# Kernel optimization log

Measured on AMD Instinct MI355X. Metric: run time of the kernel, lower is better.

Reference implementation:

```python
import jax, jax.numpy as jnp
import numpy as np

N = 50000        # num nodes
E = 800000       # num edges (before self loops)
IN = 256         # in_channels
H = 4            # heads
C = 32           # out_channels per head
NEG_SLOPE = 0.2


def _glorot(key, shape):
    fan = shape[-2] * (shape[-1] if len(shape) > 2 else 1) + shape[-1]
    # PyG glorot: uniform(-s, s) with s = sqrt(6 / (fan_in + fan_out))
    s = float(np.sqrt(6.0 / (shape[-2] + shape[-1])))
    return jax.random.uniform(key, shape, jnp.float32, -s, s)


def setup_inputs() -> dict:
    key = jax.random.key(0)
    k1, k2, k3, k4, k5 = jax.random.split(key, 5)
    x = jax.random.normal(k1, (N, IN), jnp.float32)
    src = jax.random.randint(k2, (E,), 0, N)
    dst = jax.random.randint(k3, (E,), 0, N)
    # guarantee no self loops (module removes them then re-adds exactly N loops)
    dst = jnp.where(dst == src, (dst + 1) % N, dst)
    edge_index = jnp.stack([src, dst]).astype(jnp.int32)
    weight = _glorot(k4, (IN, H * C))
    att = _glorot(k5, (1, H, 2 * C))
    bias = jnp.zeros((H * C,), jnp.float32)
    return {"x": x, "weight": weight, "att": att, "bias": bias,
            "edge_index": edge_index}


def reference(x, weight, att, bias, edge_index):
    n = x.shape[0]
    # linear projection -> [N, H, C]
    h = (x @ weight).reshape(n, H, C)
    # add self loops (input edge_index has none)
    loops = jnp.arange(n, dtype=edge_index.dtype)
    ei = jnp.concatenate([edge_index, jnp.stack([loops, loops])], axis=1)
    src, dst = ei[0], ei[1]          # flow source_to_target: j=src(row 0), i=dst(row 1)
    x_j = h[src]                     # [E', H, C] source features
    x_i = h[dst]                     # [E', H, C] target features
    wl = att[:, :, :C]               # applied to x_i (first half of concat)
    wr = att[:, :, C:]               # applied to x_j
    alpha = (x_i * wl).sum(-1) + (x_j * wr).sum(-1)   # [E', H]
    alpha = jax.nn.leaky_relu(alpha, NEG_SLOPE)
    # NOTE: module normalizes softmax over edge_index[0] (src) segments
    seg = src
    amax = jax.ops.segment_max(alpha, seg, num_segments=n)
    alpha = jnp.exp(alpha - amax[seg])
    denom = jax.ops.segment_sum(alpha, seg, num_segments=n)
    alpha = alpha / (denom[seg] + 1e-16)
    # weighted messages, aggregated at edge_index[i] = edge_index[1] (dst)
    msg = x_j * alpha[:, :, None]                     # [E', H, C]
    out = jax.ops.segment_sum(msg, dst, num_segments=n)  # [N, H, C]
    return out.reshape(n, H * C) + bias
```

## Files before the change

### kernel.cpp

```cpp
#include <hip/hip_runtime.h>
#include <hip/hip_fp16.h>
#include <math.h>


#define NH 4
#define CH 32
#define HC 128
#define IND 256
#define NEG_SLOPE 0.2f
#define CSH 8
#define NCB_MAX 256
#define CHUNK 4096

typedef __attribute__((ext_vector_type(8))) short bf16x8;
typedef __attribute__((ext_vector_type(16))) float f32x16;

__device__ __forceinline__ unsigned short f2bf(float f) {
    unsigned int u = __float_as_uint(f);
    unsigned int r = (u + 0x7FFFu + ((u >> 16) & 1u)) >> 16;
    return (unsigned short)r;
}
__device__ __forceinline__ float bf2f(unsigned short s) {
    return __uint_as_float(((unsigned int)s) << 16);
}

__global__ __launch_bounds__(256) void k_init0(int* __restrict__ histS,
                                               int* __restrict__ histD, int ncb) {
    int t = threadIdx.x;
    if (t < ncb) { histS[t] = 0; histD[t] = 0; }
}

__global__ __launch_bounds__(256) void k_wprep(const float* __restrict__ W,
                                               unsigned short* __restrict__ WT_bf) {
    int t = blockIdx.x * 256 + threadIdx.x;
    if (t >= IND * HC) return;
    int c = t >> 8;
    int k = t & 255;
    WT_bf[t] = f2bf(W[k * HC + c]);
}

__global__ __launch_bounds__(256) void k_gemm_mfma(const float* __restrict__ x,
                                                   const unsigned short* __restrict__ WT_bf,
                                                   const float* __restrict__ att,
                                                   unsigned short* __restrict__ h_bf,
                                                   float* __restrict__ al,
                                                   float* __restrict__ ar, int N) {
    __shared__ float cs[128 * 129];
    unsigned short* wsT = (unsigned short*)cs;

    const int tid  = threadIdx.x;
    const int row0 = blockIdx.x * 128;
    const int wave = tid >> 6;
    const int lane = tid & 63;
    const int n32  = lane & 31;
    const int half = lane >> 5;

    {
        int c  = tid >> 1;
        int kh = (tid & 1) * 128;
        const unsigned short* src = WT_bf + c * IND + kh;
        unsigned short* dst = wsT + c * 258 + kh;
#pragma unroll
        for (int j = 0; j < 128; j += 8)
            *(int4*)(dst + j) = *(const int4*)(src + j);
    }
    __syncthreads();

    const int row   = row0 + wave * 32 + n32;
    const bool valid = row < N;
    const float* xrow = x + (size_t)row * IND + half * 8;

    f32x16 acc[4];
#pragma unroll
    for (int t = 0; t < 4; t++)
#pragma unroll
        for (int r = 0; r < 16; r++) acc[t][r] = 0.0f;

#pragma unroll 4
    for (int s = 0; s < 16; s++) {
        float4 v0 = make_float4(0.f, 0.f, 0.f, 0.f);
        float4 v1 = v0;
        if (valid) {
            v0 = *(const float4*)(xrow + s * 16);
            v1 = *(const float4*)(xrow + s * 16 + 4);
        }
        bf16x8 a;
        a[0] = (short)f2bf(v0.x); a[1] = (short)f2bf(v0.y);
        a[2] = (short)f2bf(v0.z); a[3] = (short)f2bf(v0.w);
        a[4] = (short)f2bf(v1.x); a[5] = (short)f2bf(v1.y);
        a[6] = (short)f2bf(v1.z); a[7] = (short)f2bf(v1.w);
#pragma unroll
        for (int t = 0; t < 4; t++) {
            bf16x8 b = *(const bf16x8*)(wsT + (t * 32 + n32) * 258 + s * 16 + half * 8);
            acc[t] = __builtin_amdgcn_mfma_f32_32x32x16_bf16(a, b, acc[t], 0, 0, 0);
        }
    }
    __syncthreads();

#pragma unroll
    for (int t = 0; t < 4; t++)
#pragma unroll
        for (int r = 0; r < 16; r++) {
            int rl = wave * 32 + (r & 3) + 8 * (r >> 2) + 4 * half;
            cs[rl * 129 + t * 32 + n32] = acc[t][r];
        }
    __syncthreads();

    const int rl   = tid >> 1;
    const int chf  = tid & 1;
    const int orow = row0 + rl;
    if (orow < N) {
        const float* cr = cs + rl * 129 + chf * 64;
        unsigned short* hp = h_bf + (size_t)orow * HC + chf * 64;
#pragma unroll
        for (int c = 0; c < 64; c += 8) {
            ushort4 o0, o1;
            o0.x = f2bf(cr[c]);     o0.y = f2bf(cr[c + 1]);
            o0.z = f2bf(cr[c + 2]); o0.w = f2bf(cr[c + 3]);
            o1.x = f2bf(cr[c + 4]); o1.y = f2bf(cr[c + 5]);
            o1.z = f2bf(cr[c + 6]); o1.w = f2bf(cr[c + 7]);
            *(ushort4*)(hp + c) = o0;
            *(ushort4*)(hp + c + 4) = o1;
        }
        const int h0 = 2 * chf, h1 = 2 * chf + 1;
        const float* w0 = att + h0 * (2 * CH);
        const float* w1 = att + h1 * (2 * CH);
        float sl0 = 0.f, sr0 = 0.f, sl1 = 0.f, sr1 = 0.f;
#pragma unroll
        for (int c = 0; c < CH; c++) {
            float v0 = cr[c];
            float v1 = cr[CH + c];
            sl0 += v0 * w0[c];  sr0 += v0 * w0[CH + c];
            sl1 += v1 * w1[c];  sr1 += v1 * w1[CH + c];
        }
        al[orow * NH + h0] = sl0;  al[orow * NH + h1] = sl1;
        ar[orow * NH + h0] = sr0;  ar[orow * NH + h1] = sr1;
    }
}

__global__ __launch_bounds__(256) void k_hist(const int* __restrict__ ei,
                                              int* __restrict__ histS,
                                              int* __restrict__ histD,
                                              int E, int NE, int ncb) {
    __shared__ int hs[NCB_MAX], hd[NCB_MAX];
    hs[threadIdx.x] = 0; hd[threadIdx.x] = 0;
    __syncthreads();
    for (int t = blockIdx.x * 256 + threadIdx.x; t < NE; t += gridDim.x * 256) {
        int src, dst;
        if (t < E) { src = ei[t]; dst = ei[E + t]; }
        else       { src = dst = t - E; }
        atomicAdd(&hs[src >> CSH], 1);
        atomicAdd(&hd[dst >> CSH], 1);
    }
    __syncthreads();
    int i = threadIdx.x;
    if (i < ncb) {
        if (hs[i]) atomicAdd(&histS[i], hs[i]);
        if (hd[i]) atomicAdd(&histD[i], hd[i]);
    }
}

__global__ __launch_bounds__(256) void k_scanC(const int* __restrict__ histS,
                                               const int* __restrict__ histD,
                                               int* __restrict__ baseS,
                                               int* __restrict__ baseD,
                                               int* __restrict__ curS,
                                               int* __restrict__ curD,
                                               int* __restrict__ rowptrS,
                                               int* __restrict__ rowptrD,
                                               int ncb, int NE, int N) {
    __shared__ int sc[256];
    int tid = threadIdx.x;
    int v = (tid < ncb) ? histS[tid] : 0;
    sc[tid] = v;
    __syncthreads();
    for (int o = 1; o < 256; o <<= 1) {
        int t = (tid >= o) ? sc[tid - o] : 0;
        __syncthreads();
        sc[tid] += t;
        __syncthreads();
    }
    if (tid < ncb) { baseS[tid] = sc[tid] - v; curS[tid] = sc[tid] - v; }
    if (tid == 0) { baseS[ncb] = sc[255]; rowptrS[N] = NE; }
    __syncthreads();
    v = (tid < ncb) ? histD[tid] : 0;
    sc[tid] = v;
    __syncthreads();
    for (int o = 1; o < 256; o <<= 1) {
        int t = (tid >= o) ? sc[tid - o] : 0;
        __syncthreads();
        sc[tid] += t;
        __syncthreads();
    }
    if (tid < ncb) { baseD[tid] = sc[tid] - v; curD[tid] = sc[tid] - v; }
    if (tid == 0) { baseD[ncb] = sc[255]; rowptrD[N] = NE; }
}

__global__ __launch_bounds__(256) void k_scatterC(const int* __restrict__ ei,
                                                  int* __restrict__ gcurS,
                                                  int* __restrict__ gcurD,
                                                  unsigned int* __restrict__ recS,
                                                  unsigned int* __restrict__ recD,
                                                  int E, int NE, int ncb) {
    __shared__ unsigned int srt[CHUNK];
    __shared__ int cnt[NCB_MAX], off[NCB_MAX], cur[NCB_MAX], gpos[NCB_MAX], sc[256];
    const int tid = threadIdx.x;
    const int t0  = blockIdx.x * CHUNK;
    const int m   = min(CHUNK, NE - t0);

    unsigned int myrec[CHUNK / 256];
    int nmy = 0;
    for (int i = tid; i < m; i += 256) {
        int t = t0 + i;
        int src, dst;
        if (t < E) { src = ei[t]; dst = ei[E + t]; }
        else       { src = dst = t - E; }
        myrec[nmy++] = (unsigned int)src | ((unsigned int)dst << 16);
    }

    for (int side = 0; side < 2; side++) {
        cnt[tid] = 0;
        __syncthreads();
        int mybkt[CHUNK / 256];
        for (int k = 0; k < nmy; k++) {
            unsigned int r = myrec[k];
            int node = side ? (int)(r >> 16) : (int)(r & 0xFFFFu);
            mybkt[k] = node >> CSH;
            atomicAdd(&cnt[mybkt[k]], 1);
        }
        __syncthreads();
        int v = cnt[tid];
        sc[tid] = v;
        __syncthreads();
        for (int o = 1; o < 256; o <<= 1) {
            int t = (tid >= o) ? sc[tid - o] : 0;
            __syncthreads();
            sc[tid] += t;
            __syncthreads();
        }
        off[tid] = sc[tid] - v;
        cur[tid] = sc[tid] - v;
        __syncthreads();
        for (int k = 0; k < nmy; k++) {
            int p = atomicAdd(&cur[mybkt[k]], 1);
            srt[p] = myrec[k];
        }
        __syncthreads();
        int* gcur = side ? gcurD : gcurS;
        if (tid < ncb) {
            int c = cnt[tid];
            gpos[tid] = c ? atomicAdd(&gcur[tid], c) : 0;
        }
        __syncthreads();
        unsigned int* recX = side ? recD : recS;
        for (int i = tid; i < m; i += 256) {
            unsigned int r = srt[i];
            int node = side ? (int)(r >> 16) : (int)(r & 0xFFFFu);
            int cb = node >> CSH;
            recX[gpos[cb] + (i - off[cb])] = r;
        }
        __syncthreads();
    }
}

__global__ __launch_bounds__(256) void k_rebin(const unsigned int* __restrict__ recS,
                                               const unsigned int* __restrict__ recD,
                                               const int* __restrict__ baseS,
                                               const int* __restrict__ baseD,
                                               unsigned short* __restrict__ adjS,
                                               unsigned short* __restrict__ adjD,
                                               int* __restrict__ rowptrS,
                                               int* __restrict__ rowptrD,
                                               int ncb, int N) {
    __shared__ int cnt[256], cur[256], sc[256];
    const int tid  = threadIdx.x;
    const int side = (blockIdx.x >= ncb) ? 1 : 0;
    const int cb   = side ? blockIdx.x - ncb : blockIdx.x;
    const unsigned int* rec = side ? recD : recS;
    const int* base = side ? baseD : baseS;
    const int b0 = base[cb], b1 = base[cb + 1];
    const int tot_rec = b1 - b0;

    cnt[tid] = 0;
    __syncthreads();
    for (int i = tid; i < tot_rec; i += 256) {
        unsigned int r = rec[b0 + i];
        int node = side ? (int)(r >> 16) : (int)(r & 0xFFFFu);
        atomicAdd(&cnt[node & 255], 1);
    }
    __syncthreads();
    int v = cnt[tid];
    sc[tid] = v;
    __syncthreads();
    for (int o = 1; o < 256; o <<= 1) {
        int t = (tid >= o) ? sc[tid - o] : 0;
        __syncthreads();
        sc[tid] += t;
        __syncthreads();
    }
    int ex = sc[tid] - v;
    int node_g = (cb << CSH) + tid;
    int* rowptr = side ? rowptrD : rowptrS;
    if (node_g < N) rowptr[node_g] = b0 + ex;
    cur[tid] = ex;
    __syncthreads();
    unsigned short* adj = side ? adjD : adjS;
    for (int i = tid; i < tot_rec; i += 256) {
        unsigned int r = rec[b0 + i];
        int node = side ? (int)(r >> 16) : (int)(r & 0xFFFFu);
        unsigned short other = side ? (unsigned short)(r & 0xFFFFu)
                                    : (unsigned short)(r >> 16);
        int p = atomicAdd(&cur[node & 255], 1);
        adj[b0 + p] = other;
    }
}

__global__ __launch_bounds__(256) void k_denom(const int* __restrict__ rowptrS,
                                               const unsigned short* __restrict__ adjS,
                                               const float* __restrict__ al,
                                               const float* __restrict__ ar,
                                               float* __restrict__ rdenom, int N) {
    int n = blockIdx.x * 256 + threadIdx.x;
    if (n >= N) return;
    int beg = rowptrS[n], end = rowptrS[n + 1];
    float4 arv = *(const float4*)(ar + n * NH);
    float s0 = 0.f, s1 = 0.f, s2 = 0.f, s3 = 0.f;
    int i = beg;
    for (; i + 2 <= end; i += 2) {
        int d0 = adjS[i], d1 = adjS[i + 1];
        float4 av0 = *(const float4*)(al + d0 * NH);
        float4 av1 = *(const float4*)(al + d1 * NH);
        float a0 = av0.x + arv.x, a1 = av0.y + arv.y;
        float a2 = av0.z + arv.z, a3 = av0.w + arv.w;
        float c0 = av1.x + arv.x, c1 = av1.y + arv.y;
        float c2 = av1.z + arv.z, c3 = av1.w + arv.w;
        a0 = (a0 > 0.f) ? a0 : NEG_SLOPE * a0;
        a1 = (a1 > 0.f) ? a1 : NEG_SLOPE * a1;
        a2 = (a2 > 0.f) ? a2 : NEG_SLOPE * a2;
        a3 = (a3 > 0.f) ? a3 : NEG_SLOPE * a3;
        c0 = (c0 > 0.f) ? c0 : NEG_SLOPE * c0;
        c1 = (c1 > 0.f) ? c1 : NEG_SLOPE * c1;
        c2 = (c2 > 0.f) ? c2 : NEG_SLOPE * c2;
        c3 = (c3 > 0.f) ? c3 : NEG_SLOPE * c3;
        s0 += __expf(a0) + __expf(c0);
        s1 += __expf(a1) + __expf(c1);
        s2 += __expf(a2) + __expf(c2);
        s3 += __expf(a3) + __expf(c3);
    }
    if (i < end) {
        int d0 = adjS[i];
        float4 av = *(const float4*)(al + d0 * NH);
        float a0 = av.x + arv.x, a1 = av.y + arv.y;
        float a2 = av.z + arv.z, a3 = av.w + arv.w;
        a0 = (a0 > 0.f) ? a0 : NEG_SLOPE * a0;
        a1 = (a1 > 0.f) ? a1 : NEG_SLOPE * a1;
        a2 = (a2 > 0.f) ? a2 : NEG_SLOPE * a2;
        a3 = (a3 > 0.f) ? a3 : NEG_SLOPE * a3;
        s0 += __expf(a0); s1 += __expf(a1);
        s2 += __expf(a2); s3 += __expf(a3);
    }
    float4 r;
    r.x = 1.0f / (s0 + 1e-16f);
    r.y = 1.0f / (s1 + 1e-16f);
    r.z = 1.0f / (s2 + 1e-16f);
    r.w = 1.0f / (s3 + 1e-16f);
    *(float4*)(rdenom + n * NH) = r;
}

__global__ __launch_bounds__(256) void k_wedge(const int* __restrict__ rowptrD,
                                               const unsigned short* __restrict__ adjD,
                                               const float* __restrict__ al,
                                               const float* __restrict__ ar,
                                               const float* __restrict__ rdenom,
                                               unsigned short* __restrict__ wD, int N) {
    int n = blockIdx.x * 256 + threadIdx.x;
    if (n >= N) return;
    int beg = rowptrD[n], end = rowptrD[n + 1];
    float4 alv = *(const float4*)(al + n * NH);
    for (int i = beg; i < end; i++) {
        int s = adjD[i];
        float4 rv = *(const float4*)(ar + s * NH);
        float4 dv = *(const float4*)(rdenom + s * NH);
        float a0 = alv.x + rv.x, a1 = alv.y + rv.y;
        float a2 = alv.z + rv.z, a3 = alv.w + rv.w;
        a0 = (a0 > 0.f) ? a0 : NEG_SLOPE * a0;
        a1 = (a1 > 0.f) ? a1 : NEG_SLOPE * a1;
        a2 = (a2 > 0.f) ? a2 : NEG_SLOPE * a2;
        a3 = (a3 > 0.f) ? a3 : NEG_SLOPE * a3;
        ushort4 w;
        w.x = __half_as_ushort(__float2half(__expf(a0) * dv.x));
        w.y = __half_as_ushort(__float2half(__expf(a1) * dv.y));
        w.z = __half_as_ushort(__float2half(__expf(a2) * dv.z));
        w.w = __half_as_ushort(__float2half(__expf(a3) * dv.w));
        *(ushort4*)(wD + (size_t)i * NH) = w;
    }
}

__global__ __launch_bounds__(256) void k_agg(const int* __restrict__ rowptrD,
                                             const unsigned short* __restrict__ adjD,
                                             const unsigned short* __restrict__ wD,
                                             const unsigned short* __restrict__ h_bf,
                                             const float* __restrict__ bias,
                                             float* __restrict__ out, int N) {
    int n = blockIdx.x * 4 + (threadIdx.x >> 6);
    if (n >= N) return;
    int lane = threadIdx.x & 63;
    int c    = lane * 2;
    int hh   = lane >> 4;
    int beg = rowptrD[n], end = rowptrD[n + 1];
    float a0 = bias[c], a1 = bias[c + 1];
    float b0 = 0.f, b1 = 0.f;
    int i = beg;
    for (; i + 4 <= end; i += 4) {
        int s0 = adjD[i],     s1 = adjD[i + 1];
        int s2 = adjD[i + 2], s3 = adjD[i + 3];
        float w0 = __half2float(__ushort_as_half(wD[(size_t)i * NH + hh]));
        float w1 = __half2float(__ushort_as_half(wD[(size_t)(i + 1) * NH + hh]));
        float w2 = __half2float(__ushort_as_half(wD[(size_t)(i + 2) * NH + hh]));
        float w3 = __half2float(__ushort_as_half(wD[(size_t)(i + 3) * NH + hh]));
        ushort2 u0 = *(const ushort2*)(h_bf + (size_t)s0 * HC + c);
        ushort2 u1 = *(const ushort2*)(h_bf + (size_t)s1 * HC + c);
        ushort2 u2 = *(const ushort2*)(h_bf + (size_t)s2 * HC + c);
        ushort2 u3 = *(const ushort2*)(h_bf + (size_t)s3 * HC + c);
        a0 += bf2f(u0.x) * w0;  a1 += bf2f(u0.y) * w0;
        b0 += bf2f(u1.x) * w1;  b1 += bf2f(u1.y) * w1;
        a0 += bf2f(u2.x) * w2;  a1 += bf2f(u2.y) * w2;
        b0 += bf2f(u3.x) * w3;  b1 += bf2f(u3.y) * w3;
    }
    for (; i < end; i++) {
        int s0 = adjD[i];
        float w0 = __half2float(__ushort_as_half(wD[(size_t)i * NH + hh]));
        ushort2 u0 = *(const ushort2*)(h_bf + (size_t)s0 * HC + c);
        a0 += bf2f(u0.x) * w0;
        a1 += bf2f(u0.y) * w0;
    }
    *(float2*)(out + (size_t)n * HC + c) = make_float2(a0 + b0, a1 + b1);
}

extern "C" void kernel_launch(void* const* d_in, const int* in_sizes, int n_in,
                              void* d_out, int out_size, void* d_ws, size_t ws_size,
                              hipStream_t stream) {
    const float* x    = (const float*)d_in[0];
    const float* W    = (const float*)d_in[1];
    const float* att  = (const float*)d_in[2];
    const float* bias = (const float*)d_in[3];
    const int*   ei   = (const int*)d_in[4];

    const int N  = in_sizes[0] / IND;
    const int E  = in_sizes[4] / 2;
    const int NE = E + N;
    const int ncb = (N + (1 << CSH) - 1) >> CSH;
    float* out = (float*)d_out;
    const int nodeTot = N * NH;

    unsigned short* h_bf  = (unsigned short*)d_ws;
    unsigned short* WT_bf = h_bf + (size_t)N * HC;
    float* al      = (float*)(WT_bf + IND * HC);
    float* ar      = al + nodeTot;
    float* rdenom  = ar + nodeTot;
    unsigned int* recS = (unsigned int*)(rdenom + nodeTot);
    unsigned int* recD = recS + NE;
    unsigned short* adjS = (unsigned short*)(recD + NE);
    unsigned short* adjD = adjS + NE;
    unsigned short* wD   = adjD + NE + (NE & 1);
    int* rowptrS = (int*)(wD + (size_t)NE * NH);
    int* rowptrD = rowptrS + (N + 2);
    int* histS   = rowptrD + (N + 2);
    int* histD   = histS + NCB_MAX;
    int* baseS   = histD + NCB_MAX;
    int* baseD   = baseS + (NCB_MAX + 1);
    int* curS    = baseD + (NCB_MAX + 1);
    int* curD    = curS + NCB_MAX;

    k_init0<<<1, 256, 0, stream>>>(histS, histD, ncb);
    k_wprep<<<(IND * HC + 255) / 256, 256, 0, stream>>>(W, WT_bf);
    k_gemm_mfma<<<(N + 127) / 128, 256, 0, stream>>>(x, WT_bf, att, h_bf, al, ar, N);
    k_hist<<<256, 256, 0, stream>>>(ei, histS, histD, E, NE, ncb);
    k_scanC<<<1, 256, 0, stream>>>(histS, histD, baseS, baseD, curS, curD,
                                   rowptrS, rowptrD, ncb, NE, N);
    k_scatterC<<<(NE + CHUNK - 1) / CHUNK, 256, 0, stream>>>(ei, curS, curD,
                                                             recS, recD, E, NE, ncb);
    k_rebin<<<2 * ncb, 256, 0, stream>>>(recS, recD, baseS, baseD, adjS, adjD,
                                         rowptrS, rowptrD, ncb, N);
    k_denom<<<(N + 255) / 256, 256, 0, stream>>>(rowptrS, adjS, al, ar, rdenom, N);
    k_wedge<<<(N + 255) / 256, 256, 0, stream>>>(rowptrD, adjD, al, ar, rdenom, wD, N);
    k_agg<<<(N + 3) / 4, 256, 0, stream>>>(rowptrD, adjD, wD, h_bf, bias, out, N);
}
```

Baseline: 243.1 us.

## Fuse softmax denominator into rebin and compute edge weights inside aggregation

```diff
diff --git a/kernel.cpp b/kernel.cpp
--- a/kernel.cpp
+++ b/kernel.cpp
@@ -24,19 +24,20 @@
     return __uint_as_float(((unsigned int)s) << 16);
 }
 
-__global__ __launch_bounds__(256) void k_init0(int* __restrict__ histS,
-                                               int* __restrict__ histD, int ncb) {
-    int t = threadIdx.x;
-    if (t < ncb) { histS[t] = 0; histD[t] = 0; }
-}
-
-__global__ __launch_bounds__(256) void k_wprep(const float* __restrict__ W,
-                                               unsigned short* __restrict__ WT_bf) {
+__global__ __launch_bounds__(256) void k_prep(const float* __restrict__ W,
+                                              unsigned short* __restrict__ WT_bf,
+                                              int* __restrict__ histS,
+                                              int* __restrict__ histD, int ncb) {
     int t = blockIdx.x * 256 + threadIdx.x;
-    if (t >= IND * HC) return;
-    int c = t >> 8;
-    int k = t & 255;
-    WT_bf[t] = f2bf(W[k * HC + c]);
+    if (t < IND * HC) {
+        int c = t >> 8;
+        int k = t & 255;
+        WT_bf[t] = f2bf(W[k * HC + c]);
+    }
+    if (blockIdx.x == 0 && threadIdx.x < ncb) {
+        histS[threadIdx.x] = 0;
+        histD[threadIdx.x] = 0;
+    }
 }
 
 __global__ __launch_bounds__(256) void k_gemm_mfma(const float* __restrict__ x,
@@ -66,7 +67,7 @@
     }
     __syncthreads();
 
-    const int row   = row0 + wave * 32 + n32;
+    const int row    = row0 + wave * 32 + n32;
     const bool valid = row < N;
     const float* xrow = x + (size_t)row * IND + half * 8;
 
@@ -271,8 +272,12 @@
                                                unsigned short* __restrict__ adjD,
                                                int* __restrict__ rowptrS,
                                                int* __restrict__ rowptrD,
+                                               const float* __restrict__ al,
+                                               const float* __restrict__ ar,
+                                               float* __restrict__ rdenom,
                                                int ncb, int N) {
     __shared__ int cnt[256], cur[256], sc[256];
+    __shared__ float den[256 * NH];
     const int tid  = threadIdx.x;
     const int side = (blockIdx.x >= ncb) ? 1 : 0;
     const int cb   = side ? blockIdx.x - ncb : blockIdx.x;
@@ -282,6 +287,10 @@
     const int tot_rec = b1 - b0;
 
     cnt[tid] = 0;
+    if (side == 0) {
+#pragma unroll
+        for (int h = 0; h < NH; h++) den[tid * NH + h] = 0.f;
+    }
     __syncthreads();
     for (int i = tid; i < tot_rec; i += 256) {
         unsigned int r = rec[b0 + i];
@@ -313,126 +322,88 @@
         int p = atomicAdd(&cur[node & 255], 1);
         adj[b0 + p] = other;
     }
-}
-
-__global__ __launch_bounds__(256) void k_denom(const int* __restrict__ rowptrS,
-                                               const unsigned short* __restrict__ adjS,
-                                               const float* __restrict__ al,
-                                               const float* __restrict__ ar,
-                                               float* __restrict__ rdenom, int N) {
-    int n = blockIdx.x * 256 + threadIdx.x;
-    if (n >= N) return;
-    int beg = rowptrS[n], end = rowptrS[n + 1];
-    float4 arv = *(const float4*)(ar + n * NH);
-    float s0 = 0.f, s1 = 0.f, s2 = 0.f, s3 = 0.f;
-    int i = beg;
-    for (; i + 2 <= end; i += 2) {
-        int d0 = adjS[i], d1 = adjS[i + 1];
-        float4 av0 = *(const float4*)(al + d0 * NH);
-        float4 av1 = *(const float4*)(al + d1 * NH);
-        float a0 = av0.x + arv.x, a1 = av0.y + arv.y;
-        float a2 = av0.z + arv.z, a3 = av0.w + arv.w;
-        float c0 = av1.x + arv.x, c1 = av1.y + arv.y;
-        float c2 = av1.z + arv.z, c3 = av1.w + arv.w;
-        a0 = (a0 > 0.f) ? a0 : NEG_SLOPE * a0;
-        a1 = (a1 > 0.f) ? a1 : NEG_SLOPE * a1;
-        a2 = (a2 > 0.f) ? a2 : NEG_SLOPE * a2;
-        a3 = (a3 > 0.f) ? a3 : NEG_SLOPE * a3;
-        c0 = (c0 > 0.f) ? c0 : NEG_SLOPE * c0;
-        c1 = (c1 > 0.f) ? c1 : NEG_SLOPE * c1;
-        c2 = (c2 > 0.f) ? c2 : NEG_SLOPE * c2;
-        c3 = (c3 > 0.f) ? c3 : NEG_SLOPE * c3;
-        s0 += __expf(a0) + __expf(c0);
-        s1 += __expf(a1) + __expf(c1);
-        s2 += __expf(a2) + __expf(c2);
-        s3 += __expf(a3) + __expf(c3);
-    }
-    if (i < end) {
-        int d0 = adjS[i];
-        float4 av = *(const float4*)(al + d0 * NH);
-        float a0 = av.x + arv.x, a1 = av.y + arv.y;
-        float a2 = av.z + arv.z, a3 = av.w + arv.w;
-        a0 = (a0 > 0.f) ? a0 : NEG_SLOPE * a0;
-        a1 = (a1 > 0.f) ? a1 : NEG_SLOPE * a1;
-        a2 = (a2 > 0.f) ? a2 : NEG_SLOPE * a2;
-        a3 = (a3 > 0.f) ? a3 : NEG_SLOPE * a3;
-        s0 += __expf(a0); s1 += __expf(a1);
-        s2 += __expf(a2); s3 += __expf(a3);
-    }
-    float4 r;
-    r.x = 1.0f / (s0 + 1e-16f);
-    r.y = 1.0f / (s1 + 1e-16f);
-    r.z = 1.0f / (s2 + 1e-16f);
-    r.w = 1.0f / (s3 + 1e-16f);
-    *(float4*)(rdenom + n * NH) = r;
-}
-
-__global__ __launch_bounds__(256) void k_wedge(const int* __restrict__ rowptrD,
-                                               const unsigned short* __restrict__ adjD,
-                                               const float* __restrict__ al,
-                                               const float* __restrict__ ar,
-                                               const float* __restrict__ rdenom,
-                                               unsigned short* __restrict__ wD, int N) {
-    int n = blockIdx.x * 256 + threadIdx.x;
-    if (n >= N) return;
-    int beg = rowptrD[n], end = rowptrD[n + 1];
-    float4 alv = *(const float4*)(al + n * NH);
-    for (int i = beg; i < end; i++) {
-        int s = adjD[i];
-        float4 rv = *(const float4*)(ar + s * NH);
-        float4 dv = *(const float4*)(rdenom + s * NH);
-        float a0 = alv.x + rv.x, a1 = alv.y + rv.y;
-        float a2 = alv.z + rv.z, a3 = alv.w + rv.w;
-        a0 = (a0 > 0.f) ? a0 : NEG_SLOPE * a0;
-        a1 = (a1 > 0.f) ? a1 : NEG_SLOPE * a1;
-        a2 = (a2 > 0.f) ? a2 : NEG_SLOPE * a2;
-        a3 = (a3 > 0.f) ? a3 : NEG_SLOPE * a3;
-        ushort4 w;
-        w.x = __half_as_ushort(__float2half(__expf(a0) * dv.x));
-        w.y = __half_as_ushort(__float2half(__expf(a1) * dv.y));
-        w.z = __half_as_ushort(__float2half(__expf(a2) * dv.z));
-        w.w = __half_as_ushort(__float2half(__expf(a3) * dv.w));
-        *(ushort4*)(wD + (size_t)i * NH) = w;
+
+    if (side == 0) {
+        for (int i = tid; i < tot_rec; i += 256) {
+            unsigned int r = rec[b0 + i];
+            int src = (int)(r & 0xFFFFu);
+            int dst = (int)(r >> 16);
+            float4 av = *(const float4*)(al + dst * NH);
+            float4 rv = *(const float4*)(ar + src * NH);
+            float a0 = av.x + rv.x, a1 = av.y + rv.y;
+            float a2 = av.z + rv.z, a3 = av.w + rv.w;
+            a0 = (a0 > 0.f) ? a0 : NEG_SLOPE * a0;
+            a1 = (a1 > 0.f) ? a1 : NEG_SLOPE * a1;
+            a2 = (a2 > 0.f) ? a2 : NEG_SLOPE * a2;
+            a3 = (a3 > 0.f) ? a3 : NEG_SLOPE * a3;
+            int sl = (src & 255) * NH;
+            atomicAdd(&den[sl + 0], __expf(a0));
+            atomicAdd(&den[sl + 1], __expf(a1));
+            atomicAdd(&den[sl + 2], __expf(a2));
+            atomicAdd(&den[sl + 3], __expf(a3));
+        }
+        __syncthreads();
+        if (node_g < N) {
+            float4 r4;
+            r4.x = 1.0f / (den[tid * NH + 0] + 1e-16f);
+            r4.y = 1.0f / (den[tid * NH + 1] + 1e-16f);
+            r4.z = 1.0f / (den[tid * NH + 2] + 1e-16f);
+            r4.w = 1.0f / (den[tid * NH + 3] + 1e-16f);
+            *(float4*)(rdenom + node_g * NH) = r4;
+        }
     }
 }
 
 __global__ __launch_bounds__(256) void k_agg(const int* __restrict__ rowptrD,
                                              const unsigned short* __restrict__ adjD,
-                                             const unsigned short* __restrict__ wD,
+                                             const float* __restrict__ al,
+                                             const float* __restrict__ ar,
+                                             const float* __restrict__ rdenom,
                                              const unsigned short* __restrict__ h_bf,
                                              const float* __restrict__ bias,
                                              float* __restrict__ out, int N) {
     int n = blockIdx.x * 4 + (threadIdx.x >> 6);
     if (n >= N) return;
     int lane = threadIdx.x & 63;
+    int j    = lane & 15;
+    int hh   = lane >> 4;
     int c    = lane * 2;
-    int hh   = lane >> 4;
     int beg = rowptrD[n], end = rowptrD[n + 1];
+    float aln = al[n * NH + hh];
     float a0 = bias[c], a1 = bias[c + 1];
     float b0 = 0.f, b1 = 0.f;
-    int i = beg;
-    for (; i + 4 <= end; i += 4) {
-        int s0 = adjD[i],     s1 = adjD[i + 1];
-        int s2 = adjD[i + 2], s3 = adjD[i + 3];
-        float w0 = __half2float(__ushort_as_half(wD[(size_t)i * NH + hh]));
-        float w1 = __half2float(__ushort_as_half(wD[(size_t)(i + 1) * NH + hh]));
-        float w2 = __half2float(__ushort_as_half(wD[(size_t)(i + 2) * NH + hh]));
-        float w3 = __half2float(__ushort_as_half(wD[(size_t)(i + 3) * NH + hh]));
-        ushort2 u0 = *(const ushort2*)(h_bf + (size_t)s0 * HC + c);
-        ushort2 u1 = *(const ushort2*)(h_bf + (size_t)s1 * HC + c);
-        ushort2 u2 = *(const ushort2*)(h_bf + (size_t)s2 * HC + c);
-        ushort2 u3 = *(const ushort2*)(h_bf + (size_t)s3 * HC + c);
-        a0 += bf2f(u0.x) * w0;  a1 += bf2f(u0.y) * w0;
-        b0 += bf2f(u1.x) * w1;  b1 += bf2f(u1.y) * w1;
-        a0 += bf2f(u2.x) * w2;  a1 += bf2f(u2.y) * w2;
-        b0 += bf2f(u3.x) * w3;  b1 += bf2f(u3.y) * w3;
-    }
-    for (; i < end; i++) {
-        int s0 = adjD[i];
-        float w0 = __half2float(__ushort_as_half(wD[(size_t)i * NH + hh]));
-        ushort2 u0 = *(const ushort2*)(h_bf + (size_t)s0 * HC + c);
-        a0 += bf2f(u0.x) * w0;
-        a1 += bf2f(u0.y) * w0;
+    const int base = lane & 48;
+
+    for (int cb = beg; cb < end; cb += 16) {
+        int m = min(16, end - cb);
+        int s = 0; float w = 0.f;
+        if (j < m) {
+            s = adjD[cb + j];
+            float a = aln + ar[s * NH + hh];
+            a = (a > 0.f) ? a : NEG_SLOPE * a;
+            w = __expf(a) * rdenom[s * NH + hh];
+        }
+        int sk[16]; float wk[16];
+#pragma unroll
+        for (int k = 0; k < 16; k++) {
+            if (k < m) {
+                sk[k] = __shfl(s, base + k);
+                wk[k] = __shfl(w, base + k);
+            } else { sk[k] = 0; wk[k] = 0.f; }
+        }
+#pragma unroll
+        for (int k = 0; k < 16; k += 2) {
+            if (k < m) {
+                ushort2 u = *(const ushort2*)(h_bf + (size_t)sk[k] * HC + c);
+                a0 += bf2f(u.x) * wk[k];
+                a1 += bf2f(u.y) * wk[k];
+            }
+            if (k + 1 < m) {
+                ushort2 u = *(const ushort2*)(h_bf + (size_t)sk[k + 1] * HC + c);
+                b0 += bf2f(u.x) * wk[k + 1];
+                b1 += bf2f(u.y) * wk[k + 1];
+            }
+        }
     }
     *(float2*)(out + (size_t)n * HC + c) = make_float2(a0 + b0, a1 + b1);
 }
@@ -462,8 +433,7 @@
     unsigned int* recD = recS + NE;
     unsigned short* adjS = (unsigned short*)(recD + NE);
     unsigned short* adjD = adjS + NE;
-    unsigned short* wD   = adjD + NE + (NE & 1);
-    int* rowptrS = (int*)(wD + (size_t)NE * NH);
+    int* rowptrS = (int*)(adjD + NE + (NE & 1));
     int* rowptrD = rowptrS + (N + 2);
     int* histS   = rowptrD + (N + 2);
     int* histD   = histS + NCB_MAX;
@@ -472,8 +442,7 @@
     int* curS    = baseD + (NCB_MAX + 1);
     int* curD    = curS + NCB_MAX;
 
-    k_init0<<<1, 256, 0, stream>>>(histS, histD, ncb);
-    k_wprep<<<(IND * HC + 255) / 256, 256, 0, stream>>>(W, WT_bf);
+    k_prep<<<128, 256, 0, stream>>>(W, WT_bf, histS, histD, ncb);
     k_gemm_mfma<<<(N + 127) / 128, 256, 0, stream>>>(x, WT_bf, att, h_bf, al, ar, N);
     k_hist<<<256, 256, 0, stream>>>(ei, histS, histD, E, NE, ncb);
     k_scanC<<<1, 256, 0, stream>>>(histS, histD, baseS, baseD, curS, curD,
@@ -481,8 +450,7 @@
     k_scatterC<<<(NE + CHUNK - 1) / CHUNK, 256, 0, stream>>>(ei, curS, curD,
                                                              recS, recD, E, NE, ncb);
     k_rebin<<<2 * ncb, 256, 0, stream>>>(recS, recD, baseS, baseD, adjS, adjD,
-                                         rowptrS, rowptrD, ncb, N);
-    k_denom<<<(N + 255) / 256, 256, 0, stream>>>(rowptrS, adjS, al, ar, rdenom, N);
-    k_wedge<<<(N + 255) / 256, 256, 0, stream>>>(rowptrD, adjD, al, ar, rdenom, wD, N);
-    k_agg<<<(N + 3) / 4, 256, 0, stream>>>(rowptrD, adjD, wD, h_bf, bias, out, N);
-}
+                                         rowptrS, rowptrD, al, ar, rdenom, ncb, N);
+    k_agg<<<(N + 3) / 4, 256, 0, stream>>>(rowptrD, adjD, al, ar, rdenom,
+                                           h_bf, bias, out, N);
+}
```

After: 267.1 us. 9.9% more time.
